# Kernel optimization log

Hardware: AMD Instinct MI355X
Metric: run time of the kernel (lower is better)

## Reference

```python
import jax, jax.numpy as jnp
import numpy as np

B, D, H, HD, P, O, K = 256, 1024, 8, 128, 2048, 1024, 4
HID = H * HD
EPS = 1e-5


def setup_inputs() -> dict:
    key = jax.random.key(0)
    ks = jax.random.split(key, 16)

    def w(k, shape, fan_in):
        return jax.random.normal(k, shape, jnp.float32) / np.sqrt(fan_in).astype(np.float32)

    return dict(
        seq=jax.random.normal(ks[0], (B, D), jnp.float32),
        c_tm1=jnp.zeros((B, H, HD, HD), jnp.float32),
        n_tm1=jnp.ones((B, H, HD), jnp.float32),
        m_tm1=jnp.zeros((B, H), jnp.float32),
        ln_g=jnp.ones((D,), jnp.float32), ln_b=jnp.zeros((D,), jnp.float32),
        gn_g=jnp.ones((HID,), jnp.float32), gn_b=jnp.zeros((HID,), jnp.float32),
        W_upl=w(ks[1], (P, D), D), b_upl=jnp.zeros((P,), jnp.float32),
        W_upr=w(ks[2], (HID, D), D), b_upr=jnp.zeros((HID,), jnp.float32),
        W_down=w(ks[3], (D, HID), HID), b_down=jnp.zeros((D,), jnp.float32),
        W_last=w(ks[4], (O, D), D), b_last=jnp.zeros((O,), jnp.float32),
        conv_w=w(ks[5], (K,), K), conv_b=jnp.zeros((), jnp.float32),
        W_skip=w(ks[6], (HID, P), P),
        W_i=w(ks[7], (H, P), P), b_i=jnp.zeros((H,), jnp.float32),
        W_f=w(ks[8], (H, P), P), b_f=jnp.zeros((H,), jnp.float32),
        W_o=w(ks[9], (HID, P), P), b_o=jnp.zeros((HID,), jnp.float32),
        W_q=w(ks[10], (HID, P), P), b_q=jnp.zeros((HID,), jnp.float32),
        W_k=w(ks[11], (HID, P), P), b_k=jnp.zeros((HID,), jnp.float32),
        W_v=w(ks[12], (HID, P), P), b_v=jnp.zeros((HID,), jnp.float32),
    )


def reference(seq, c_tm1, n_tm1, m_tm1, ln_g, ln_b, gn_g, gn_b,
              W_upl, b_upl, W_upr, b_upr, W_down, b_down, W_last, b_last,
              conv_w, conv_b, W_skip, W_i, b_i, W_f, b_f, W_o, b_o,
              W_q, b_q, W_k, b_k, W_v, b_v):
    b = seq.shape[0]
    h, hd = c_tm1.shape[1], c_tm1.shape[2]

    # input LayerNorm
    mu = jnp.mean(seq, -1, keepdims=True)
    var = jnp.var(seq, -1, keepdims=True)
    x_n = (seq - mu) * jax.lax.rsqrt(var + EPS) * ln_g + ln_b

    x_t = x_n @ W_upl.T + b_upl            # [b, P]
    r_t = x_n @ W_upr.T + b_upr            # [b, HID]

    # causal conv over the feature axis (in=out=1 channel), left pad K-1
    k_sz = conv_w.shape[0]
    p = x_t.shape[1]
    xp = jnp.pad(x_t, ((0, 0), (k_sz - 1, 0)))
    x_c = conv_b + sum(conv_w[j] * xp[:, j:j + p] for j in range(k_sz))
    x_c = jax.nn.silu(x_c)                 # [b, P]

    q_t = (x_c @ W_q.T + b_q).reshape(b, h, hd)
    k_t = ((x_c @ W_k.T + b_k) / np.sqrt(hd).astype(np.float32)).reshape(b, h, hd)
    v_t = (x_t @ W_v.T + b_v).reshape(b, h, hd)

    i_t = x_c @ W_i.T + b_i                # [b, h]
    f_t = x_c @ W_f.T + b_f                # [b, h]
    o_t = jax.nn.sigmoid(x_t @ W_o.T + b_o)  # [b, HID]

    # stabilized exponential gating
    m_t = jnp.maximum(f_t + m_tm1, i_t)
    i_g = jnp.exp(i_t - m_t)
    f_g = jnp.exp(f_t - m_t + m_tm1)

    # matrix-memory covariance update
    c_t = f_g[:, :, None, None] * c_tm1 + i_g[:, :, None, None] * jnp.einsum('bhd,bhp->bhdp', v_t, k_t)
    n_t = f_g[:, :, None] * n_tm1 + i_g[:, :, None] * k_t

    num = jnp.einsum('bhdp,bhp->bhd', c_t, q_t)
    den = jnp.maximum(jnp.einsum('bhd,bhd->bh', n_t, q_t), 1.0)
    h_t = o_t * (num / den[:, :, None]).reshape(b, h * hd)

    # GroupNorm(head_num groups) over hidden
    hg = h_t.reshape(b, h, hd)
    gmu = jnp.mean(hg, -1, keepdims=True)
    gvar = jnp.var(hg, -1, keepdims=True)
    hn = ((hg - gmu) * jax.lax.rsqrt(gvar + EPS)).reshape(b, h * hd) * gn_g + gn_b

    out = hn + x_c @ W_skip.T              # 1x1 conv skip == matmul
    out = out * jax.nn.silu(r_t)
    out = out @ W_down.T + b_down
    final = (out + x_n) @ W_last.T + b_last
    return final, c_t, n_t, m_t
```

## Files before the change

kernel.cpp:

```cpp
#include <hip/hip_runtime.h>
#include <cstdint>
#include <cstddef>

#define LN_EPS 1e-5f

typedef float  f32x4  __attribute__((ext_vector_type(4)));
typedef __bf16 bf16x8 __attribute__((ext_vector_type(8)));
typedef unsigned short u16x4 __attribute__((ext_vector_type(4)));

__device__ __forceinline__ float block_sum(float v, volatile float* red) {
#pragma unroll
  for (int o = 32; o > 0; o >>= 1) v += __shfl_down(v, o, 64);
  const int lane = threadIdx.x & 63, w = threadIdx.x >> 6;
  __syncthreads();
  if (lane == 0) red[w] = v;
  __syncthreads();
  return red[0] + red[1] + red[2] + red[3];
}

__global__ __launch_bounds__(256)
void k_ln(const float* __restrict__ seq, const float* __restrict__ g,
          const float* __restrict__ b, float* __restrict__ xn) {
  __shared__ float red[8];
  const int row = blockIdx.x, t = threadIdx.x;
  const f32x4 x = ((const f32x4*)(seq + (size_t)row * 1024))[t];
  float s  = x[0] + x[1] + x[2] + x[3];
  float s2 = x[0]*x[0] + x[1]*x[1] + x[2]*x[2] + x[3]*x[3];
#pragma unroll
  for (int o = 32; o > 0; o >>= 1) { s += __shfl_down(s, o, 64); s2 += __shfl_down(s2, o, 64); }
  const int lane = t & 63, w = t >> 6;
  if (lane == 0) { red[w] = s; red[4 + w] = s2; }
  __syncthreads();
  s  = red[0] + red[1] + red[2] + red[3];
  s2 = red[4] + red[5] + red[6] + red[7];
  const float mu  = s * (1.f / 1024.f);
  const float inv = rsqrtf(s2 * (1.f / 1024.f) - mu * mu + LN_EPS);
  const f32x4 gg = ((const f32x4*)g)[t];
  const f32x4 bb = ((const f32x4*)b)[t];
  f32x4 y;
#pragma unroll
  for (int i = 0; i < 4; ++i) y[i] = (x[i] - mu) * inv * gg[i] + bb[i];
  ((f32x4*)(xn + (size_t)row * 1024))[t] = y;
}

__global__ __launch_bounds__(256)
void k_conv(const float* __restrict__ xt, const float* __restrict__ cw,
            const float* __restrict__ cb, float* __restrict__ xc) {
  __shared__ float s[2048];
  const int row = blockIdx.x, t = threadIdx.x;
  const f32x4* src = (const f32x4*)(xt + (size_t)row * 2048);
  ((f32x4*)s)[t] = src[t];
  ((f32x4*)s)[t + 256] = src[t + 256];
  const float w0 = cw[0], w1 = cw[1], w2 = cw[2], w3 = cw[3], b = cb[0];
  __syncthreads();
  float out[8];
  const int c0 = t * 8;
#pragma unroll
  for (int j = 0; j < 8; ++j) {
    const int c = c0 + j;
    float a = b + w3 * s[c];
    if (c >= 1) a += w2 * s[c - 1];
    if (c >= 2) a += w1 * s[c - 2];
    if (c >= 3) a += w0 * s[c - 3];
    a = a / (1.f + __expf(-a));
    out[j] = a;
  }
  f32x4* dst = (f32x4*)(xc + (size_t)row * 2048 + c0);
  f32x4 v0 = {out[0], out[1], out[2], out[3]};
  f32x4 v1 = {out[4], out[5], out[6], out[7]};
  dst[0] = v0; dst[1] = v1;
}

__global__ __launch_bounds__(256)
void k_if(const float* __restrict__ xc, const float* __restrict__ Wi,
          const float* __restrict__ bi, const float* __restrict__ Wf,
          const float* __restrict__ bfp, const float* __restrict__ m_tm1,
          float* __restrict__ m_out, float* __restrict__ ig, float* __restrict__ fg) {
  __shared__ float sx[2048];
  __shared__ float so[16];
  const int row = blockIdx.x, t = threadIdx.x;
  const f32x4* src = (const f32x4*)(xc + (size_t)row * 2048);
  ((f32x4*)sx)[t] = src[t];
  ((f32x4*)sx)[t + 256] = src[t + 256];
  __syncthreads();
  const int w = t >> 6, lane = t & 63;
  float p[4];
#pragma unroll
  for (int i = 0; i < 4; ++i) {
    const int o = w * 4 + i;
    const float* wr = (o < 8) ? (Wi + (size_t)o * 2048) : (Wf + (size_t)(o - 8) * 2048);
    float acc = 0.f;
#pragma unroll
    for (int j = 0; j < 8; ++j) {
      const f32x4 xv = ((const f32x4*)sx)[j * 64 + lane];
      const f32x4 wv = ((const f32x4*)wr)[j * 64 + lane];
      acc += xv[0]*wv[0] + xv[1]*wv[1] + xv[2]*wv[2] + xv[3]*wv[3];
    }
    p[i] = acc;
  }
#pragma unroll
  for (int i = 0; i < 4; ++i) {
#pragma unroll
    for (int o = 32; o > 0; o >>= 1) p[i] += __shfl_xor(p[i], o, 64);
  }
  if (lane == 0) {
#pragma unroll
    for (int i = 0; i < 4; ++i) so[w * 4 + i] = p[i];
  }
  __syncthreads();
  if (t < 8) {
    const float it = so[t] + bi[t];
    const float ft = so[t + 8] + bfp[t];
    const float mp = m_tm1[row * 8 + t];
    const float m = fmaxf(ft + mp, it);
    m_out[row * 8 + t] = m;
    ig[row * 8 + t] = __expf(it - m);
    fg[row * 8 + t] = __expf(ft - m + mp);
  }
}

__global__ __launch_bounds__(256)
void k_rec(const float* __restrict__ c_tm1, const float* __restrict__ n_tm1,
           const float* __restrict__ qb, const float* __restrict__ kb,
           const float* __restrict__ vb, const float* __restrict__ ot,
           const float* __restrict__ ig, const float* __restrict__ fg,
           const float* __restrict__ gn_g, const float* __restrict__ gn_b,
           const float* __restrict__ skipb, const float* __restrict__ sr,
           float* __restrict__ c_out, float* __restrict__ n_out,
           float* __restrict__ uf) {
  __shared__ float sk[128], sq[128], sv[128], snum[128];
  __shared__ float red[4];
  const int bh = blockIdx.x;
  const int b = bh >> 3, h = bh & 7;
  const int t = threadIdx.x;
  const size_t base = (size_t)b * 1024 + h * 128;
  if (t < 128) { sk[t] = kb[base + t]; sv[t] = vb[base + t]; }
  else         { sq[t - 128] = qb[base + t - 128]; }
  __syncthreads();
  const float fgv = fg[bh], igv = ig[bh];
  const float* C0 = c_tm1 + (size_t)bh * 16384;
  float* Ct = c_out + (size_t)bh * 16384;
  const int r0 = t >> 5, c4 = t & 31;
  const f32x4 k4 = ((const f32x4*)sk)[c4];
  const f32x4 q4 = ((const f32x4*)sq)[c4];
  float pd[16];
#pragma unroll
  for (int pass = 0; pass < 16; ++pass) {
    const int d = pass * 8 + r0;
    const f32x4 c0v = ((const f32x4*)C0)[d * 32 + c4];
    const float iv = igv * sv[d];
    f32x4 ct = fgv * c0v + iv * k4;
    __builtin_nontemporal_store(ct, ((f32x4*)Ct) + d * 32 + c4);
    pd[pass] = ct[0] * q4[0] + ct[1] * q4[1] + ct[2] * q4[2] + ct[3] * q4[3];
  }
#pragma unroll
  for (int pass = 0; pass < 16; ++pass) {
    float p = pd[pass];
    p += __shfl_xor(p, 1, 64); p += __shfl_xor(p, 2, 64); p += __shfl_xor(p, 4, 64);
    p += __shfl_xor(p, 8, 64); p += __shfl_xor(p, 16, 64);
    pd[pass] = p;
  }
  if (c4 == 0) {
#pragma unroll
    for (int pass = 0; pass < 16; ++pass) snum[pass * 8 + r0] = pd[pass];
  }
  float denp = 0.f, ntd = 0.f;
  if (t < 128) {
    ntd = fgv * n_tm1[(size_t)bh * 128 + t] + igv * sk[t];
    n_out[(size_t)bh * 128 + t] = ntd;
    denp = ntd * sq[t];
  }
  const float den = fmaxf(block_sum(denp, red), 1.f);
  float hv = 0.f;
  if (t < 128) {
    const float o = 1.f / (1.f + __expf(-ot[base + t]));
    hv = o * snum[t] / den;
  }
  const float mu  = block_sum(hv, red) * (1.f / 128.f);
  const float var = block_sum(hv * hv, red) * (1.f / 128.f) - mu * mu;
  if (t < 128) {
    const int hid = h * 128 + t;
    const float hn = (hv - mu) * rsqrtf(var + LN_EPS) * gn_g[hid] + gn_b[hid];
    uf[base + t] = (hv - mu) * 0.f + (hn + skipb[base + t]) * sr[base + t];
  }
}

struct GemmSeg {
  const float* A; const float* W; const float* bias; float* out;
  const float* add; int ldOut; int colOfs; int epi; float scale;
};
struct GemmArgs { GemmSeg seg[5]; };

__global__ __launch_bounds__(256)
void k_gemm(int K, GemmArgs ga) {
  __shared__ __align__(16) char lds[2][32768];
  const int tid = threadIdx.x;
  const int lane = tid & 63;
  const int wid = tid >> 6;
  const int wm = wid >> 1;
  const int wn = wid & 1;
  const int segId = blockIdx.x >> 4;
  const int n0 = (blockIdx.x & 15) * 64;
  const int m0 = blockIdx.y * 64;
  const GemmSeg sg = ga.seg[segId];

  const int lrow = tid >> 4;
  const int col4 = tid & 15;

  f32x4 acc[2][2] = {};

  const float* Abase = sg.A + (size_t)m0 * K;
  const float* Wbase = sg.W + (size_t)n0 * K;
  const int NT = K >> 6;

  f32x4 va[4], vw[4], va2[4], vw2[4];
#pragma unroll
  for (int p = 0; p < 4; ++p) {
    const int r = p * 16 + lrow;
    va[p] = *(const f32x4*)(Abase + (size_t)r * K + col4 * 4);
    vw[p] = *(const f32x4*)(Wbase + (size_t)r * K + col4 * 4);
  }

  for (int kt = 0; kt < NT; ++kt) {
    {
      char* lb = lds[kt & 1];
      const int byte = ((((col4 >> 1) ^ (lrow & 7)) << 4) | ((col4 & 1) << 3));
#pragma unroll
      for (int p = 0; p < 4; ++p) {
        const int r = p * 16 + lrow;
        u16x4 ah, al, wh, wl;
#pragma unroll
        for (int i = 0; i < 4; ++i) {
          const unsigned ab = __float_as_uint(va[p][i]);
          const float fh = __uint_as_float(ab & 0xFFFF0000u);
          ah[i] = (unsigned short)(ab >> 16);
          al[i] = (unsigned short)(__float_as_uint(va[p][i] - fh) >> 16);
          const unsigned wb2 = __float_as_uint(vw[p][i]);
          const float wfh = __uint_as_float(wb2 & 0xFFFF0000u);
          wh[i] = (unsigned short)(wb2 >> 16);
          wl[i] = (unsigned short)(__float_as_uint(vw[p][i] - wfh) >> 16);
        }
        *(u16x4*)(lb + r * 128 + byte) = ah;
        *(u16x4*)(lb + 8192 + r * 128 + byte) = al;
        *(u16x4*)(lb + 16384 + r * 128 + byte) = wh;
        *(u16x4*)(lb + 24576 + r * 128 + byte) = wl;
      }
    }
    if (kt + 1 < NT) {
      const int ko = (kt + 1) * 64;
#pragma unroll
      for (int p = 0; p < 4; ++p) {
        const int r = p * 16 + lrow;
        va2[p] = *(const f32x4*)(Abase + (size_t)r * K + ko + col4 * 4);
        vw2[p] = *(const f32x4*)(Wbase + (size_t)r * K + ko + col4 * 4);
      }
    }
    __syncthreads();
    {
      const char* lb = lds[kt & 1];
      const int rA = wm * 32 + (lane & 15);
      const int rB = wn * 32 + (lane & 15);
      const int kg = lane >> 4;
      const int swz = lane & 7;
#pragma unroll
      for (int kk = 0; kk < 2; ++kk) {
        const int so = ((kk * 4 + kg) ^ swz) << 4;
        const char* pa0 = lb + rA * 128 + so;
        const char* pa1 = lb + (rA + 16) * 128 + so;
        const char* pb0 = lb + 16384 + rB * 128 + so;
        const char* pb1 = lb + 16384 + (rB + 16) * 128 + so;
        const bf16x8 ah0 = *(const bf16x8*)(pa0);
        const bf16x8 al0 = *(const bf16x8*)(pa0 + 8192);
        const bf16x8 ah1 = *(const bf16x8*)(pa1);
        const bf16x8 al1 = *(const bf16x8*)(pa1 + 8192);
        const bf16x8 bh0 = *(const bf16x8*)(pb0);
        const bf16x8 bl0 = *(const bf16x8*)(pb0 + 8192);
        const bf16x8 bh1 = *(const bf16x8*)(pb1);
        const bf16x8 bl1 = *(const bf16x8*)(pb1 + 8192);
        acc[0][0] = __builtin_amdgcn_mfma_f32_16x16x32_bf16(ah0, bh0, acc[0][0], 0, 0, 0);
        acc[0][1] = __builtin_amdgcn_mfma_f32_16x16x32_bf16(ah0, bh1, acc[0][1], 0, 0, 0);
        acc[1][0] = __builtin_amdgcn_mfma_f32_16x16x32_bf16(ah1, bh0, acc[1][0], 0, 0, 0);
        acc[1][1] = __builtin_amdgcn_mfma_f32_16x16x32_bf16(ah1, bh1, acc[1][1], 0, 0, 0);
        acc[0][0] = __builtin_amdgcn_mfma_f32_16x16x32_bf16(ah0, bl0, acc[0][0], 0, 0, 0);
        acc[0][1] = __builtin_amdgcn_mfma_f32_16x16x32_bf16(ah0, bl1, acc[0][1], 0, 0, 0);
        acc[1][0] = __builtin_amdgcn_mfma_f32_16x16x32_bf16(ah1, bl0, acc[1][0], 0, 0, 0);
        acc[1][1] = __builtin_amdgcn_mfma_f32_16x16x32_bf16(ah1, bl1, acc[1][1], 0, 0, 0);
        acc[0][0] = __builtin_amdgcn_mfma_f32_16x16x32_bf16(al0, bh0, acc[0][0], 0, 0, 0);
        acc[0][1] = __builtin_amdgcn_mfma_f32_16x16x32_bf16(al0, bh1, acc[0][1], 0, 0, 0);
        acc[1][0] = __builtin_amdgcn_mfma_f32_16x16x32_bf16(al1, bh0, acc[1][0], 0, 0, 0);
        acc[1][1] = __builtin_amdgcn_mfma_f32_16x16x32_bf16(al1, bh1, acc[1][1], 0, 0, 0);
      }
    }
#pragma unroll
    for (int p = 0; p < 4; ++p) { va[p] = va2[p]; vw[p] = vw2[p]; }
    __syncthreads();
  }

  const int rowb = m0 + wm * 32 + (lane >> 4) * 4;
  const int colb = n0 + wn * 32 + (lane & 15);
#pragma unroll
  for (int mf = 0; mf < 2; ++mf) {
#pragma unroll
    for (int nf = 0; nf < 2; ++nf) {
      const int col = colb + nf * 16;
      const float bv = sg.bias ? sg.bias[col] : 0.f;
#pragma unroll
      for (int i = 0; i < 4; ++i) {
        const int row = rowb + mf * 16 + i;
        float v = acc[mf][nf][i] + bv;
        if (sg.epi == 1)      v = v / (1.f + __expf(-v));
        else if (sg.epi == 3) v *= sg.scale;
        else if (sg.epi == 4) v += sg.add[(size_t)row * 1024 + col];
        sg.out[(size_t)row * sg.ldOut + sg.colOfs + col] = v;
      }
    }
  }
}

extern "C" void kernel_launch(void* const* d_in, const int* in_sizes, int n_in,
                              void* d_out, int out_size, void* d_ws, size_t ws_size,
                              hipStream_t stream) {
  (void)in_sizes; (void)n_in; (void)out_size; (void)ws_size;
  const float* seq    = (const float*)d_in[0];
  const float* c_tm1  = (const float*)d_in[1];
  const float* n_tm1  = (const float*)d_in[2];
  const float* m_tm1  = (const float*)d_in[3];
  const float* ln_g   = (const float*)d_in[4];
  const float* ln_b   = (const float*)d_in[5];
  const float* gn_g   = (const float*)d_in[6];
  const float* gn_b   = (const float*)d_in[7];
  const float* W_upl  = (const float*)d_in[8];
  const float* b_upl  = (const float*)d_in[9];
  const float* W_upr  = (const float*)d_in[10];
  const float* b_upr  = (const float*)d_in[11];
  const float* W_down = (const float*)d_in[12];
  const float* b_down = (const float*)d_in[13];
  const float* W_last = (const float*)d_in[14];
  const float* b_last = (const float*)d_in[15];
  const float* conv_w = (const float*)d_in[16];
  const float* conv_b = (const float*)d_in[17];
  const float* W_skip = (const float*)d_in[18];
  const float* W_i    = (const float*)d_in[19];
  const float* b_i    = (const float*)d_in[20];
  const float* W_f    = (const float*)d_in[21];
  const float* b_f    = (const float*)d_in[22];
  const float* W_o    = (const float*)d_in[23];
  const float* b_o    = (const float*)d_in[24];
  const float* W_q    = (const float*)d_in[25];
  const float* b_q    = (const float*)d_in[26];
  const float* W_k    = (const float*)d_in[27];
  const float* b_k    = (const float*)d_in[28];
  const float* W_v    = (const float*)d_in[29];
  const float* b_v    = (const float*)d_in[30];

  float* out_final = (float*)d_out;
  float* out_c = out_final + (size_t)256 * 1024;
  float* out_n = out_c + (size_t)256 * 8 * 128 * 128;
  float* out_m = out_n + (size_t)256 * 8 * 128;

  char* ws = (char*)d_ws;
  size_t off = 0;
  auto alloc = [&](size_t bytes) -> void* {
    void* p = ws + off; off += (bytes + 255) & ~(size_t)255; return p;
  };
  float* x_n   = (float*)alloc((size_t)256 * 1024 * 4);
  float* x_t   = (float*)alloc((size_t)256 * 2048 * 4);
  float* sr    = (float*)alloc((size_t)256 * 1024 * 4);
  float* x_c   = (float*)alloc((size_t)256 * 2048 * 4);
  float* qb    = (float*)alloc((size_t)256 * 1024 * 4);
  float* kb    = (float*)alloc((size_t)256 * 1024 * 4);
  float* vb    = (float*)alloc((size_t)256 * 1024 * 4);
  float* otb   = (float*)alloc((size_t)256 * 1024 * 4);
  float* skipb = (float*)alloc((size_t)256 * 1024 * 4);
  float* igb   = (float*)alloc((size_t)2048 * 4);
  float* fgb   = (float*)alloc((size_t)2048 * 4);
  float* u_f   = (float*)alloc((size_t)256 * 1024 * 4);
  float* t_f   = (float*)alloc((size_t)256 * 1024 * 4);

  k_ln<<<256, 256, 0, stream>>>(seq, ln_g, ln_b, x_n);

  GemmArgs gA = {};
  gA.seg[0] = {x_n, W_upl, b_upl, x_t, nullptr, 2048, 0, 0, 0.f};
  gA.seg[1] = {x_n, W_upl + (size_t)1024 * 1024, b_upl + 1024, x_t, nullptr, 2048, 1024, 0, 0.f};
  gA.seg[2] = {x_n, W_upr, b_upr, sr, nullptr, 1024, 0, 1, 0.f};
  k_gemm<<<dim3(48, 4), 256, 0, stream>>>(1024, gA);

  k_conv<<<256, 256, 0, stream>>>(x_t, conv_w, conv_b, x_c);

  k_if<<<256, 256, 0, stream>>>(x_c, W_i, b_i, W_f, b_f, m_tm1, out_m, igb, fgb);

  GemmArgs gBC = {};
  gBC.seg[0] = {x_c, W_q, b_q, qb, nullptr, 1024, 0, 0, 0.f};
  gBC.seg[1] = {x_c, W_k, b_k, kb, nullptr, 1024, 0, 3, 0.08838834764831845f};
  gBC.seg[2] = {x_c, W_skip, nullptr, skipb, nullptr, 1024, 0, 0, 0.f};
  gBC.seg[3] = {x_t, W_v, b_v, vb, nullptr, 1024, 0, 0, 0.f};
  gBC.seg[4] = {x_t, W_o, b_o, otb, nullptr, 1024, 0, 0, 0.f};
  k_gemm<<<dim3(80, 4), 256, 0, stream>>>(2048, gBC);

  k_rec<<<2048, 256, 0, stream>>>(c_tm1, n_tm1, qb, kb, vb, otb, igb, fgb,
                                  gn_g, gn_b, skipb, sr, out_c, out_n, u_f);

  GemmArgs gD = {};
  gD.seg[0] = {u_f, W_down, b_down, t_f, x_n, 1024, 0, 4, 0.f};
  k_gemm<<<dim3(16, 4), 256, 0, stream>>>(1024, gD);

  GemmArgs gE = {};
  gE.seg[0] = {t_f, W_last, b_last, out_final, nullptr, 1024, 0, 0, 0.f};
  k_gemm<<<dim3(16, 4), 256, 0, stream>>>(1024, gE);
}
```

Before: 162.3 us.

## Split recurrence kernel into streaming C-update and per-head finalize kernels

The fused recurrence kernel, which had one block per (batch, head) stream over a 64 KB C matrix, is split in two. A streaming kernel now uses four blocks per head, each handling 32 rows with loads issued up front, and writes the q-dot products to a global scratch buffer. A small 128-thread finalize kernel then computes n_t, the denominator, the GroupNorm and the skip/gate epilogue. This is meant to raise memory-level parallelism and occupancy on the bandwidth-bound C update, at the cost of an extra launch and a small global round trip for num.

```diff
diff --git a/kernel.cpp b/kernel.cpp
--- a/kernel.cpp
+++ b/kernel.cpp
@@ -120,69 +120,83 @@
 }
 
 __global__ __launch_bounds__(256)
-void k_rec(const float* __restrict__ c_tm1, const float* __restrict__ n_tm1,
-           const float* __restrict__ qb, const float* __restrict__ kb,
-           const float* __restrict__ vb, const float* __restrict__ ot,
-           const float* __restrict__ ig, const float* __restrict__ fg,
-           const float* __restrict__ gn_g, const float* __restrict__ gn_b,
-           const float* __restrict__ skipb, const float* __restrict__ sr,
-           float* __restrict__ c_out, float* __restrict__ n_out,
-           float* __restrict__ uf) {
-  __shared__ float sk[128], sq[128], sv[128], snum[128];
-  __shared__ float red[4];
-  const int bh = blockIdx.x;
+void k_rec_stream(const float* __restrict__ c_tm1, const float* __restrict__ kb,
+                  const float* __restrict__ qb, const float* __restrict__ vb,
+                  const float* __restrict__ ig, const float* __restrict__ fg,
+                  float* __restrict__ c_out, float* __restrict__ numG) {
+  const int blk = blockIdx.x;
+  const int bh = blk >> 2;
+  const int rg = blk & 3;
+  const int t = threadIdx.x;
+  const int w = t >> 6, lane = t & 63;
+  const int c4 = lane & 31;
+  const int half = lane >> 5;
   const int b = bh >> 3, h = bh & 7;
-  const int t = threadIdx.x;
-  const size_t base = (size_t)b * 1024 + h * 128;
-  if (t < 128) { sk[t] = kb[base + t]; sv[t] = vb[base + t]; }
-  else         { sq[t - 128] = qb[base + t - 128]; }
-  __syncthreads();
+  const size_t vecbase = (size_t)b * 1024 + h * 128;
   const float fgv = fg[bh], igv = ig[bh];
-  const float* C0 = c_tm1 + (size_t)bh * 16384;
-  float* Ct = c_out + (size_t)bh * 16384;
-  const int r0 = t >> 5, c4 = t & 31;
-  const f32x4 k4 = ((const f32x4*)sk)[c4];
-  const f32x4 q4 = ((const f32x4*)sq)[c4];
-  float pd[16];
-#pragma unroll
-  for (int pass = 0; pass < 16; ++pass) {
-    const int d = pass * 8 + r0;
-    const f32x4 c0v = ((const f32x4*)C0)[d * 32 + c4];
-    const float iv = igv * sv[d];
-    f32x4 ct = fgv * c0v + iv * k4;
-    __builtin_nontemporal_store(ct, ((f32x4*)Ct) + d * 32 + c4);
-    pd[pass] = ct[0] * q4[0] + ct[1] * q4[1] + ct[2] * q4[2] + ct[3] * q4[3];
-  }
-#pragma unroll
-  for (int pass = 0; pass < 16; ++pass) {
-    float p = pd[pass];
+  const f32x4 k4 = ((const f32x4*)(kb + vecbase))[c4];
+  const f32x4 q4 = ((const f32x4*)(qb + vecbase))[c4];
+  const int row0 = rg * 32 + w * 8;
+  const f32x4* C0 = (const f32x4*)(c_tm1 + (size_t)bh * 16384);
+  f32x4* Ct = (f32x4*)(c_out + (size_t)bh * 16384);
+  f32x4 c0s[4]; float vrow[4];
+#pragma unroll
+  for (int j = 0; j < 4; ++j) {
+    const int r = row0 + 2 * j + half;
+    c0s[j] = C0[r * 32 + c4];
+    vrow[j] = vb[vecbase + r];
+  }
+  float pd[4];
+#pragma unroll
+  for (int j = 0; j < 4; ++j) {
+    const int r = row0 + 2 * j + half;
+    const float iv = igv * vrow[j];
+    f32x4 ct = fgv * c0s[j] + iv * k4;
+    __builtin_nontemporal_store(ct, Ct + r * 32 + c4);
+    pd[j] = ct[0] * q4[0] + ct[1] * q4[1] + ct[2] * q4[2] + ct[3] * q4[3];
+  }
+#pragma unroll
+  for (int j = 0; j < 4; ++j) {
+    float p = pd[j];
     p += __shfl_xor(p, 1, 64); p += __shfl_xor(p, 2, 64); p += __shfl_xor(p, 4, 64);
     p += __shfl_xor(p, 8, 64); p += __shfl_xor(p, 16, 64);
-    pd[pass] = p;
-  }
-  if (c4 == 0) {
-#pragma unroll
-    for (int pass = 0; pass < 16; ++pass) snum[pass * 8 + r0] = pd[pass];
-  }
-  float denp = 0.f, ntd = 0.f;
-  if (t < 128) {
-    ntd = fgv * n_tm1[(size_t)bh * 128 + t] + igv * sk[t];
-    n_out[(size_t)bh * 128 + t] = ntd;
-    denp = ntd * sq[t];
-  }
-  const float den = fmaxf(block_sum(denp, red), 1.f);
-  float hv = 0.f;
-  if (t < 128) {
-    const float o = 1.f / (1.f + __expf(-ot[base + t]));
-    hv = o * snum[t] / den;
-  }
-  const float mu  = block_sum(hv, red) * (1.f / 128.f);
-  const float var = block_sum(hv * hv, red) * (1.f / 128.f) - mu * mu;
-  if (t < 128) {
-    const int hid = h * 128 + t;
-    const float hn = (hv - mu) * rsqrtf(var + LN_EPS) * gn_g[hid] + gn_b[hid];
-    uf[base + t] = (hv - mu) * 0.f + (hn + skipb[base + t]) * sr[base + t];
-  }
+    if (c4 == 0) numG[(size_t)bh * 128 + row0 + 2 * j + half] = p;
+  }
+}
+
+__device__ __forceinline__ float bsum128(float v, volatile float* red) {
+#pragma unroll
+  for (int o = 32; o > 0; o >>= 1) v += __shfl_xor(v, o, 64);
+  const int w = threadIdx.x >> 6;
+  __syncthreads();
+  if ((threadIdx.x & 63) == 0) red[w] = v;
+  __syncthreads();
+  return red[0] + red[1];
+}
+
+__global__ __launch_bounds__(128)
+void k_rec_fin(const float* __restrict__ n_tm1, const float* __restrict__ kb,
+               const float* __restrict__ qb, const float* __restrict__ ot,
+               const float* __restrict__ ig, const float* __restrict__ fg,
+               const float* __restrict__ numG,
+               const float* __restrict__ gn_g, const float* __restrict__ gn_b,
+               const float* __restrict__ skipb, const float* __restrict__ sr,
+               float* __restrict__ n_out, float* __restrict__ uf) {
+  __shared__ float red[2];
+  const int bh = blockIdx.x, t = threadIdx.x;
+  const int b = bh >> 3, h = bh & 7;
+  const size_t base = (size_t)b * 1024 + h * 128;
+  const float fgv = fg[bh], igv = ig[bh];
+  const float ntd = fgv * n_tm1[(size_t)bh * 128 + t] + igv * kb[base + t];
+  n_out[(size_t)bh * 128 + t] = ntd;
+  const float den = fmaxf(bsum128(ntd * qb[base + t], red), 1.f);
+  const float o = 1.f / (1.f + __expf(-ot[base + t]));
+  const float hv = o * numG[(size_t)bh * 128 + t] / den;
+  const float mu  = bsum128(hv, red) * (1.f / 128.f);
+  const float var = bsum128(hv * hv, red) * (1.f / 128.f) - mu * mu;
+  const int hid = h * 128 + t;
+  const float hn = (hv - mu) * rsqrtf(var + LN_EPS) * gn_g[hid] + gn_b[hid];
+  uf[base + t] = (hn + skipb[base + t]) * sr[base + t];
 }
 
 struct GemmSeg {
@@ -376,6 +390,7 @@
   float* fgb   = (float*)alloc((size_t)2048 * 4);
   float* u_f   = (float*)alloc((size_t)256 * 1024 * 4);
   float* t_f   = (float*)alloc((size_t)256 * 1024 * 4);
+  float* numG  = (float*)alloc((size_t)2048 * 128 * 4);
 
   k_ln<<<256, 256, 0, stream>>>(seq, ln_g, ln_b, x_n);
 
@@ -397,8 +412,10 @@
   gBC.seg[4] = {x_t, W_o, b_o, otb, nullptr, 1024, 0, 0, 0.f};
   k_gemm<<<dim3(80, 4), 256, 0, stream>>>(2048, gBC);
 
-  k_rec<<<2048, 256, 0, stream>>>(c_tm1, n_tm1, qb, kb, vb, otb, igb, fgb,
-                                  gn_g, gn_b, skipb, sr, out_c, out_n, u_f);
+  k_rec_stream<<<8192, 256, 0, stream>>>(c_tm1, kb, qb, vb, igb, fgb, out_c, numG);
+
+  k_rec_fin<<<2048, 128, 0, stream>>>(n_tm1, kb, qb, otb, igb, fgb, numG,
+                                      gn_g, gn_b, skipb, sr, out_n, u_f);
 
   GemmArgs gD = {};
   gD.seg[0] = {u_f, W_down, b_down, t_f, x_n, 1024, 0, 4, 0.f};
```

Result: no change. 163.4 us (+0.7%).
